# Kernel optimization log

Hardware: AMD Instinct MI355X
Metric: run time of the kernel (lower is better)

Reference implementation:

```python
import jax, jax.numpy as jnp
import numpy as np

N_NODES = 50000
N_EDGES = 800000
D = 128
E_DIM = 32
N_LAYERS = 4
BN_EPS = 1e-5


def setup_inputs() -> dict:
    key = jax.random.key(0)
    ks = jax.random.split(key, 9)
    return {
        "x": jax.random.normal(ks[0], (N_NODES, D), dtype=jnp.float32),
        "edge_attr": jax.random.normal(ks[1], (N_EDGES, E_DIM), dtype=jnp.float32),
        "edge_index": jax.random.randint(ks[2], (2, N_EDGES), 0, N_NODES, dtype=jnp.int64),
        "W_edge": jax.random.normal(ks[3], (N_LAYERS, E_DIM, D), dtype=jnp.float32) * 0.1,
        "b_edge": jnp.zeros((N_LAYERS, D), dtype=jnp.float32),
        "W1": jax.random.normal(ks[4], (N_LAYERS, D, D), dtype=jnp.float32) * 0.1,
        "b1": jnp.zeros((N_LAYERS, D), dtype=jnp.float32),
        "W2": jax.random.normal(ks[5], (N_LAYERS, D, D), dtype=jnp.float32) * 0.1,
        "b2": jnp.zeros((N_LAYERS, D), dtype=jnp.float32),
        "gamma": jnp.ones((N_LAYERS, D), dtype=jnp.float32),
        "beta": jnp.zeros((N_LAYERS, D), dtype=jnp.float32),
    }


def reference(x, edge_attr, edge_index, W_edge, b_edge, W1, b1, W2, b2, gamma, beta):
    src, dst = edge_index[0], edge_index[1]
    n = x.shape[0]
    for i in range(N_LAYERS):
        # GINEConv: message = ReLU(x_src + Lin(edge_attr)); scatter-add to dst
        e = edge_attr @ W_edge[i] + b_edge[i]            # [E, D]
        m = jax.nn.relu(x[src] + e)                      # [E, D]
        agg = jax.ops.segment_sum(m, dst, num_segments=n)  # [N, D]
        h = x + agg                                      # (1+eps)*x, eps=0
        # 2-layer MLP
        h = jax.nn.relu(h @ W1[i] + b1[i]) @ W2[i] + b2[i]
        # BatchNorm (training-mode batch stats, biased var) + ReLU; dropout off
        mean = h.mean(axis=0)
        var = h.var(axis=0)
        h = (h - mean) * jax.lax.rsqrt(var + BN_EPS) * gamma[i] + beta[i]
        x = jax.nn.relu(h)
    return x
```

## Files before the change

kernel.cpp:

```cpp
#include <hip/hip_runtime.h>

#define NN 50000
#define NE 800000
#define DD 128
#define ED 32
#define NL 4
#define BN_EPS 1e-5f
#define SCAN_B 1024
#define NB ((NN + SCAN_B - 1) / SCAN_B)
#define EB 128
#define MR 32

typedef __attribute__((ext_vector_type(8))) short bf16x8;
typedef __attribute__((ext_vector_type(4))) float f32x4;

__device__ __forceinline__ unsigned short f2bf(float f) {
    unsigned u = __float_as_uint(f);
    u += 0x7fffu + ((u >> 16) & 1u);
    return (unsigned short)(u >> 16);
}
__device__ __forceinline__ float bf2f(unsigned short h) {
    return __uint_as_float((unsigned)h << 16);
}

__global__ __launch_bounds__(256) void hist_kernel(
    const int* __restrict__ edst, int* __restrict__ deg)
{
    const int e = blockIdx.x * 256 + threadIdx.x;
    if (e < NE) atomicAdd(&deg[edst[e]], 1);
}

__global__ __launch_bounds__(256) void scan1_kernel(
    const int* __restrict__ deg, int* __restrict__ rowptr, int* __restrict__ bsum)
{
    __shared__ int sh[256];
    const int t = threadIdx.x, b = blockIdx.x;
    const int base = b * SCAN_B + t * 4;
    int v[4];
#pragma unroll
    for (int j = 0; j < 4; ++j) {
        const int idx = base + j;
        v[j] = (idx < NN) ? deg[idx] : 0;
    }
    sh[t] = v[0] + v[1] + v[2] + v[3];
    __syncthreads();
    for (int off = 1; off < 256; off <<= 1) {
        const int val = (t >= off) ? sh[t - off] : 0;
        __syncthreads();
        sh[t] += val;
        __syncthreads();
    }
    int p = (t == 0) ? 0 : sh[t - 1];
#pragma unroll
    for (int j = 0; j < 4; ++j) {
        const int idx = base + j;
        if (idx < NN) rowptr[idx] = p;
        p += v[j];
    }
    if (t == 255) bsum[b] = sh[255];
}

__global__ void scan2_kernel(int* __restrict__ bsum)
{
    if (threadIdx.x == 0) {
        int acc = 0;
        for (int i = 0; i < NB; ++i) { const int v = bsum[i]; bsum[i] = acc; acc += v; }
    }
}

__global__ __launch_bounds__(256) void scan3_kernel(
    int* __restrict__ rowptr, int* __restrict__ cursor, const int* __restrict__ bsum)
{
    const int idx = blockIdx.x * 256 + threadIdx.x;
    if (idx < NN) {
        const int v = rowptr[idx] + bsum[idx / SCAN_B];
        rowptr[idx] = v;
        cursor[idx] = v;
    }
    if (idx == 0) rowptr[NN] = NE;
}

__global__ __launch_bounds__(256) void scatter_idx_kernel(
    const int* __restrict__ edst, int* __restrict__ cursor, int* __restrict__ eid_perm)
{
    const int e = blockIdx.x * 256 + threadIdx.x;
    if (e < NE) {
        const int pos = atomicAdd(&cursor[edst[e]], 1);
        eid_perm[pos] = e;
    }
}

__global__ __launch_bounds__(256) void sdfill_kernel(
    const int* __restrict__ rowptr, const int* __restrict__ eid_perm,
    const int* __restrict__ esrc, int2* __restrict__ sd_perm)
{
    const int d = blockIdx.x * 256 + threadIdx.x;
    if (d < NN) {
        const int b = rowptr[d], e = rowptr[d + 1];
        for (int p = b; p < e; ++p)
            sd_perm[p] = make_int2(esrc[eid_perm[p]], d);
    }
}

__global__ __launch_bounds__(256) void ea_gather_kernel(
    const float* __restrict__ ea, const int* __restrict__ eid_perm,
    unsigned short* __restrict__ ea_bf)
{
    const int tid = blockIdx.x * 256 + threadIdx.x;
    const int pos = tid >> 3, j = tid & 7;
    if (pos < NE) {
        const int e = eid_perm[pos];
        const float4 v = *(const float4*)&ea[(size_t)e * ED + j * 4];
        uint2 p;
        p.x = (unsigned)f2bf(v.x) | ((unsigned)f2bf(v.y) << 16);
        p.y = (unsigned)f2bf(v.z) | ((unsigned)f2bf(v.w) << 16);
        *(uint2*)&ea_bf[(size_t)pos * ED + j * 4] = p;
    }
}

__global__ __launch_bounds__(256) void x0conv_kernel(
    const float* __restrict__ x0, unsigned short* __restrict__ xbf)
{
    const size_t i = ((size_t)blockIdx.x * 256 + threadIdx.x) * 8;
    if (i >= (size_t)NN * DD) return;
    const float4 a = *(const float4*)&x0[i];
    const float4 b = *(const float4*)&x0[i + 4];
    uint4 o;
    o.x = (unsigned)f2bf(a.x) | ((unsigned)f2bf(a.y) << 16);
    o.y = (unsigned)f2bf(a.z) | ((unsigned)f2bf(a.w) << 16);
    o.z = (unsigned)f2bf(b.x) | ((unsigned)f2bf(b.y) << 16);
    o.w = (unsigned)f2bf(b.z) | ((unsigned)f2bf(b.w) << 16);
    *(uint4*)&xbf[i] = o;
}

__global__ __launch_bounds__(256) void wconv_kernel(
    const float* __restrict__ We, unsigned short* __restrict__ wtb)
{
    const int tid = blockIdx.x * 256 + threadIdx.x;
    if (tid < NL * DD * ED) {
        const int l = tid / (DD * ED);
        const int r = tid % (DD * ED);
        const int c = r / ED, k = r % ED;
        wtb[tid] = f2bf(We[(size_t)l * ED * DD + k * DD + c]);
    }
}

__global__ __launch_bounds__(256) void w12conv_kernel(
    const float* __restrict__ W1, const float* __restrict__ W2,
    unsigned short* __restrict__ w1t, unsigned short* __restrict__ w2t)
{
    const int tid = blockIdx.x * 256 + threadIdx.x;
    if (tid < NL * DD * DD) {
        const int l = tid / (DD * DD);
        const int r = tid % (DD * DD);
        const int n = r / DD, k = r % DD;
        const size_t s = (size_t)l * DD * DD + k * DD + n;
        w1t[tid] = f2bf(W1[s]);
        w2t[tid] = f2bf(W2[s]);
    }
}

__global__ __launch_bounds__(256, 5) void edge_mfma_kernel(
    const unsigned short* __restrict__ xbf,
    const unsigned short* __restrict__ eab,
    const int2* __restrict__ sd_perm,
    const unsigned short* __restrict__ wtb,
    const float* __restrict__ be,
    float* __restrict__ agg)
{
    __shared__ unsigned short msgl[EB * 128];
    const int t = threadIdx.x;
    const int wv = t >> 6, ln = t & 63;
    const int l15 = ln & 15, kb = ln >> 4;
    const int e0 = blockIdx.x * EB;

    const int c0 = (2 * wv + 0) * 16 + l15;
    const int c1 = (2 * wv + 1) * 16 + l15;
    const bf16x8 bfr0 = *(const bf16x8*)&wtb[c0 * ED + kb * 8];
    const bf16x8 bfr1 = *(const bf16x8*)&wtb[c1 * ED + kb * 8];

#pragma unroll
    for (int eg = 0; eg < EB / 16; ++eg) {
        const int edge = eg * 16 + l15;
        const bf16x8 afr = *(const bf16x8*)&eab[(size_t)(e0 + edge) * ED + kb * 8];
        f32x4 z = {0.f, 0.f, 0.f, 0.f};
        const f32x4 d0 = __builtin_amdgcn_mfma_f32_16x16x32_bf16(afr, bfr0, z, 0, 0, 0);
        const f32x4 d1 = __builtin_amdgcn_mfma_f32_16x16x32_bf16(afr, bfr1, z, 0, 0, 0);
#pragma unroll
        for (int j = 0; j < 4; ++j) {
            const int mrow = eg * 16 + kb * 4 + j;
            const int sw = ((mrow >> 2) & 3) << 3;
            const int i0 = (((c0 >> 1) ^ sw) << 1) | (c0 & 1);
            const int i1 = (((c1 >> 1) ^ sw) << 1) | (c1 & 1);
            msgl[mrow * 128 + i0] = f2bf(d0[j]);
            msgl[mrow * 128 + i1] = f2bf(d1[j]);
        }
    }
    __syncthreads();

    const int lbase = wv * 32;
    const int2* sdp = &sd_perm[e0 + lbase];
    const int c2 = ln * 2;
    const float2 bv = *(const float2*)&be[c2];
    float2 acc = {0.f, 0.f};
    int seg_start = 0;
#pragma unroll 1
    for (int g = 0; g < 2; ++g) {
        const int gb = g * 16;
        int4 pr[8];
#pragma unroll
        for (int q = 0; q < 8; ++q)
            pr[q] = *(const int4*)&sdp[gb + 2 * q];
        int srcs[16], dsts[17];
#pragma unroll
        for (int q = 0; q < 8; ++q) {
            srcs[2 * q] = pr[q].x; srcs[2 * q + 1] = pr[q].z;
            dsts[2 * q] = pr[q].y; dsts[2 * q + 1] = pr[q].w;
        }
        dsts[16] = (gb + 16 < 32) ? sdp[gb + 16].y : -1;
        float2 xv[16];
#pragma unroll
        for (int q = 0; q < 16; ++q) {
            const unsigned xu = *(const unsigned*)&xbf[(size_t)srcs[q] * DD + c2];
            xv[q].x = __uint_as_float(xu << 16);
            xv[q].y = __uint_as_float(xu & 0xffff0000u);
        }
#pragma unroll
        for (int q = 0; q < 16; ++q) {
            const int i = gb + q;
            const int dw = ln ^ (((i >> 2) & 3) << 3);
            const unsigned mm = *(const unsigned*)&msgl[(lbase + i) * 128 + dw * 2];
            const float mlo = __uint_as_float(mm << 16);
            const float mhi = __uint_as_float(mm & 0xffff0000u);
            acc.x += fmaxf(xv[q].x + mlo + bv.x, 0.f);
            acc.y += fmaxf(xv[q].y + mhi + bv.y, 0.f);
            if (i == 31 || dsts[q + 1] != dsts[q]) {
                float* ap = &agg[(size_t)dsts[q] * DD + c2];
                if (seg_start > 0 && i < 31) {
                    *(float2*)ap = acc;
                } else {
                    unsafeAtomicAdd(ap + 0, acc.x);
                    unsafeAtomicAdd(ap + 1, acc.y);
                }
                acc.x = 0.f; acc.y = 0.f;
                seg_start = i + 1;
            }
        }
    }
}

__global__ __launch_bounds__(256, 5) void mlp_mfma_kernel(
    const unsigned short* __restrict__ xbf, const float* __restrict__ agg,
    float* __restrict__ h2out,
    const unsigned short* __restrict__ w1t,
    const unsigned short* __restrict__ w2t,
    const float* __restrict__ b1, const float* __restrict__ b2,
    float* __restrict__ bns)
{
    __shared__ unsigned short ah[MR * 128];
    __shared__ unsigned short al[MR * 128];
    __shared__ unsigned short bh[MR * 128];
    __shared__ unsigned short bl[MR * 128];
    const int t = threadIdx.x;
    const int wv = t >> 6, ln = t & 63, l15 = ln & 15, kb = ln >> 4;
    const int r0 = blockIdx.x * MR;

#pragma unroll
    for (int p = 0; p < 2; ++p) {
        const int row = p * 16 + (t >> 4);
        const int gc = t & 15;
        const int grow = r0 + row;
        float v[8] = {0.f, 0.f, 0.f, 0.f, 0.f, 0.f, 0.f, 0.f};
        if (grow < NN) {
            const size_t g = (size_t)grow * DD + gc * 8;
            const uint4 xu = *(const uint4*)&xbf[g];
            const float4 ga = *(const float4*)&agg[g];
            const float4 gb4 = *(const float4*)&agg[g + 4];
            v[0] = __uint_as_float(xu.x << 16)          + ga.x;
            v[1] = __uint_as_float(xu.x & 0xffff0000u)  + ga.y;
            v[2] = __uint_as_float(xu.y << 16)          + ga.z;
            v[3] = __uint_as_float(xu.y & 0xffff0000u)  + ga.w;
            v[4] = __uint_as_float(xu.z << 16)          + gb4.x;
            v[5] = __uint_as_float(xu.z & 0xffff0000u)  + gb4.y;
            v[6] = __uint_as_float(xu.w << 16)          + gb4.z;
            v[7] = __uint_as_float(xu.w & 0xffff0000u)  + gb4.w;
        }
        unsigned hiw[4], low[4];
#pragma unroll
        for (int j = 0; j < 4; ++j) {
            const unsigned short h0 = f2bf(v[2 * j]);
            const unsigned short h1 = f2bf(v[2 * j + 1]);
            const unsigned short q0 = f2bf(v[2 * j] - bf2f(h0));
            const unsigned short q1 = f2bf(v[2 * j + 1] - bf2f(h1));
            hiw[j] = (unsigned)h0 | ((unsigned)h1 << 16);
            low[j] = (unsigned)q0 | ((unsigned)q1 << 16);
        }
        const int off = row * 128 + (gc ^ (row & 7)) * 8;
        *(uint4*)&ah[off] = *(uint4*)hiw;
        *(uint4*)&al[off] = *(uint4*)low;
    }

    bf16x8 w1f[2][4];
#pragma unroll
    for (int nt = 0; nt < 2; ++nt) {
        const int n = wv * 32 + nt * 16 + l15;
#pragma unroll
        for (int ks = 0; ks < 4; ++ks)
            w1f[nt][ks] = *(const bf16x8*)&w1t[n * DD + ks * 32 + kb * 8];
    }
    const int cA = wv * 32 + l15, cB = wv * 32 + 16 + l15;
    const float b1v[2] = {b1[cA], b1[cB]};
    const float b2v[2] = {b2[cA], b2[cB]};
    __syncthreads();

    f32x4 acc[2][2];
#pragma unroll
    for (int mt = 0; mt < 2; ++mt)
#pragma unroll
        for (int nt = 0; nt < 2; ++nt)
            acc[mt][nt] = (f32x4){0.f, 0.f, 0.f, 0.f};
#pragma unroll
    for (int ks = 0; ks < 4; ++ks) {
#pragma unroll
        for (int mt = 0; mt < 2; ++mt) {
            const int row = mt * 16 + l15;
            const int off = row * 128 + ((ks * 4 + kb) ^ (row & 7)) * 8;
            const bf16x8 afh = *(const bf16x8*)&ah[off];
            const bf16x8 afl = *(const bf16x8*)&al[off];
#pragma unroll
            for (int nt = 0; nt < 2; ++nt) {
                acc[mt][nt] = __builtin_amdgcn_mfma_f32_16x16x32_bf16(afh, w1f[nt][ks], acc[mt][nt], 0, 0, 0);
                acc[mt][nt] = __builtin_amdgcn_mfma_f32_16x16x32_bf16(afl, w1f[nt][ks], acc[mt][nt], 0, 0, 0);
            }
        }
    }

#pragma unroll
    for (int mt = 0; mt < 2; ++mt) {
#pragma unroll
        for (int nt = 0; nt < 2; ++nt) {
            const int col = wv * 32 + nt * 16 + l15;
#pragma unroll
            for (int j = 0; j < 4; ++j) {
                const int row = mt * 16 + kb * 4 + j;
                const float v = fmaxf(acc[mt][nt][j] + b1v[nt], 0.f);
                const unsigned short hi = f2bf(v);
                const int off = row * 128 + ((col >> 3) ^ (row & 7)) * 8 + (col & 7);
                bh[off] = hi;
                bl[off] = f2bf(v - bf2f(hi));
            }
        }
    }

    bf16x8 w2f[2][4];
#pragma unroll
    for (int nt = 0; nt < 2; ++nt) {
        const int n = wv * 32 + nt * 16 + l15;
#pragma unroll
        for (int ks = 0; ks < 4; ++ks)
            w2f[nt][ks] = *(const bf16x8*)&w2t[n * DD + ks * 32 + kb * 8];
    }
    __syncthreads();

#pragma unroll
    for (int mt = 0; mt < 2; ++mt)
#pragma unroll
        for (int nt = 0; nt < 2; ++nt)
            acc[mt][nt] = (f32x4){0.f, 0.f, 0.f, 0.f};
#pragma unroll
    for (int ks = 0; ks < 4; ++ks) {
#pragma unroll
        for (int mt = 0; mt < 2; ++mt) {
            const int row = mt * 16 + l15;
            const int off = row * 128 + ((ks * 4 + kb) ^ (row & 7)) * 8;
            const bf16x8 afh = *(const bf16x8*)&bh[off];
            const bf16x8 afl = *(const bf16x8*)&bl[off];
#pragma unroll
            for (int nt = 0; nt < 2; ++nt) {
                acc[mt][nt] = __builtin_amdgcn_mfma_f32_16x16x32_bf16(afh, w2f[nt][ks], acc[mt][nt], 0, 0, 0);
                acc[mt][nt] = __builtin_amdgcn_mfma_f32_16x16x32_bf16(afl, w2f[nt][ks], acc[mt][nt], 0, 0, 0);
            }
        }
    }

    float ps[2] = {0.f, 0.f}, pq[2] = {0.f, 0.f};
#pragma unroll
    for (int mt = 0; mt < 2; ++mt) {
#pragma unroll
        for (int nt = 0; nt < 2; ++nt) {
            const int col = wv * 32 + nt * 16 + l15;
#pragma unroll
            for (int j = 0; j < 4; ++j) {
                const int row = r0 + mt * 16 + kb * 4 + j;
                const float v = acc[mt][nt][j] + b2v[nt];
                if (row < NN) {
                    h2out[(size_t)row * DD + col] = v;
                    ps[nt] += v;
                    pq[nt] += v * v;
                }
            }
        }
    }
#pragma unroll
    for (int nt = 0; nt < 2; ++nt) {
        ps[nt] += __shfl_xor(ps[nt], 16);
        ps[nt] += __shfl_xor(ps[nt], 32);
        pq[nt] += __shfl_xor(pq[nt], 16);
        pq[nt] += __shfl_xor(pq[nt], 32);
    }
    if (kb == 0) {
#pragma unroll
        for (int nt = 0; nt < 2; ++nt) {
            const int col = wv * 32 + nt * 16 + l15;
            unsafeAtomicAdd(&bns[col], ps[nt]);
            unsafeAtomicAdd(&bns[DD + col], pq[nt]);
        }
    }
}

__global__ __launch_bounds__(256) void bn_apply_bf16(
    float* __restrict__ h2, const float* __restrict__ bns,
    const float* __restrict__ gamma, const float* __restrict__ beta,
    unsigned short* __restrict__ xout)
{
    const size_t i = ((size_t)blockIdx.x * 256 + threadIdx.x) * 4;
    if (i >= (size_t)NN * DD) return;
    const int c4 = (int)(i & 127);
    const float4 hv = *(const float4*)&h2[i];
    const float4 sv = *(const float4*)&bns[c4];
    const float4 qv = *(const float4*)&bns[DD + c4];
    const float4 gv = *(const float4*)&gamma[c4];
    const float4 bv = *(const float4*)&beta[c4];
    const float inv_n = 1.f / (float)NN;
    float o0, o1, o2, o3;
    { const float m = sv.x * inv_n; const float var = qv.x * inv_n - m * m;
      o0 = fmaxf((hv.x - m) * __frsqrt_rn(var + BN_EPS) * gv.x + bv.x, 0.f); }
    { const float m = sv.y * inv_n; const float var = qv.y * inv_n - m * m;
      o1 = fmaxf((hv.y - m) * __frsqrt_rn(var + BN_EPS) * gv.y + bv.y, 0.f); }
    { const float m = sv.z * inv_n; const float var = qv.z * inv_n - m * m;
      o2 = fmaxf((hv.z - m) * __frsqrt_rn(var + BN_EPS) * gv.z + bv.z, 0.f); }
    { const float m = sv.w * inv_n; const float var = qv.w * inv_n - m * m;
      o3 = fmaxf((hv.w - m) * __frsqrt_rn(var + BN_EPS) * gv.w + bv.w, 0.f); }
    uint2 o;
    o.x = (unsigned)f2bf(o0) | ((unsigned)f2bf(o1) << 16);
    o.y = (unsigned)f2bf(o2) | ((unsigned)f2bf(o3) << 16);
    *(uint2*)&xout[i] = o;
    *(float4*)&h2[i] = (float4){0.f, 0.f, 0.f, 0.f};
}

__global__ __launch_bounds__(256) void bn_apply_f32(
    const float* __restrict__ h2, const float* __restrict__ bns,
    const float* __restrict__ gamma, const float* __restrict__ beta,
    float* __restrict__ xout)
{
    const size_t i = ((size_t)blockIdx.x * 256 + threadIdx.x) * 4;
    if (i >= (size_t)NN * DD) return;
    const int c4 = (int)(i & 127);
    const float4 hv = *(const float4*)&h2[i];
    const float4 sv = *(const float4*)&bns[c4];
    const float4 qv = *(const float4*)&bns[DD + c4];
    const float4 gv = *(const float4*)&gamma[c4];
    const float4 bv = *(const float4*)&beta[c4];
    const float inv_n = 1.f / (float)NN;
    float4 ov;
    { const float m = sv.x * inv_n; const float var = qv.x * inv_n - m * m;
      ov.x = fmaxf((hv.x - m) * __frsqrt_rn(var + BN_EPS) * gv.x + bv.x, 0.f); }
    { const float m = sv.y * inv_n; const float var = qv.y * inv_n - m * m;
      ov.y = fmaxf((hv.y - m) * __frsqrt_rn(var + BN_EPS) * gv.y + bv.y, 0.f); }
    { const float m = sv.z * inv_n; const float var = qv.z * inv_n - m * m;
      ov.z = fmaxf((hv.z - m) * __frsqrt_rn(var + BN_EPS) * gv.z + bv.z, 0.f); }
    { const float m = sv.w * inv_n; const float var = qv.w * inv_n - m * m;
      ov.w = fmaxf((hv.w - m) * __frsqrt_rn(var + BN_EPS) * gv.w + bv.w, 0.f); }
    *(float4*)&xout[i] = ov;
}

extern "C" void kernel_launch(void* const* d_in, const int* in_sizes, int n_in,
                              void* d_out, int out_size, void* d_ws, size_t ws_size,
                              hipStream_t stream) {
    const float* x0    = (const float*)d_in[0];
    const float* ea    = (const float*)d_in[1];
    const int*   eidx  = (const int*)d_in[2];
    const float* We    = (const float*)d_in[3];
    const float* be    = (const float*)d_in[4];
    const float* W1    = (const float*)d_in[5];
    const float* b1    = (const float*)d_in[6];
    const float* W2    = (const float*)d_in[7];
    const float* b2    = (const float*)d_in[8];
    const float* gamma = (const float*)d_in[9];
    const float* beta  = (const float*)d_in[10];
    float* out = (float*)d_out;
    float* ws  = (float*)d_ws;

    float* agg = ws;
    float* bns = agg + (size_t)NN * DD;
    int* deg      = (int*)(bns + NL * 256);
    int* rowptr   = deg + 50000;
    int* cursor   = rowptr + 50004;
    int* bsum     = cursor + 50000;
    int2* sd_perm = (int2*)(bsum + 64);
    int* eid_perm = (int*)(sd_perm + NE);
    unsigned short* ea_bf = (unsigned short*)(eid_perm + NE);
    unsigned short* wt_bf = ea_bf + (size_t)NE * ED;
    unsigned short* w1t   = wt_bf + (size_t)NL * DD * ED;
    unsigned short* w2t   = w1t + (size_t)NL * DD * DD;
    unsigned short* xbf   = w2t + (size_t)NL * DD * DD;

    const int* esrc = eidx;
    const int* edst = eidx + NE;

    hipMemsetAsync(deg, 0, NN * sizeof(int), stream);
    hipMemsetAsync(bns, 0, NL * 256 * sizeof(float), stream);
    hipMemsetAsync(agg, 0, (size_t)NN * DD * sizeof(float), stream);
    hist_kernel<<<(NE + 255) / 256, 256, 0, stream>>>(edst, deg);
    scan1_kernel<<<NB, 256, 0, stream>>>(deg, rowptr, bsum);
    scan2_kernel<<<1, 64, 0, stream>>>(bsum);
    scan3_kernel<<<(NN + 255) / 256, 256, 0, stream>>>(rowptr, cursor, bsum);
    scatter_idx_kernel<<<(NE + 255) / 256, 256, 0, stream>>>(edst, cursor, eid_perm);
    sdfill_kernel<<<(NN + 255) / 256, 256, 0, stream>>>(rowptr, eid_perm, esrc, sd_perm);
    ea_gather_kernel<<<(NE * 8 + 255) / 256, 256, 0, stream>>>(ea, eid_perm, ea_bf);
    x0conv_kernel<<<((NN * DD / 8) + 255) / 256, 256, 0, stream>>>(x0, xbf);
    wconv_kernel<<<(NL * DD * ED + 255) / 256, 256, 0, stream>>>(We, wt_bf);
    w12conv_kernel<<<(NL * DD * DD + 255) / 256, 256, 0, stream>>>(W1, W2, w1t, w2t);

    for (int l = 0; l < NL; ++l) {
        edge_mfma_kernel<<<NE / EB, 256, 0, stream>>>(
            xbf, ea_bf, sd_perm,
            wt_bf + (size_t)l * DD * ED, be + (size_t)l * DD, agg);
        mlp_mfma_kernel<<<(NN + MR - 1) / MR, 256, 0, stream>>>(
            xbf, agg, agg,
            w1t + (size_t)l * DD * DD, w2t + (size_t)l * DD * DD,
            b1 + (size_t)l * DD, b2 + (size_t)l * DD, bns + l * 256);
        if (l < NL - 1) {
            bn_apply_bf16<<<(NN * DD / 4 + 255) / 256, 256, 0, stream>>>(
                agg, bns + l * 256, gamma + (size_t)l * DD, beta + (size_t)l * DD, xbf);
        } else {
            bn_apply_f32<<<(NN * DD / 4 + 255) / 256, 256, 0, stream>>>(
                agg, bns + l * 256, gamma + (size_t)l * DD, beta + (size_t)l * DD, out);
        }
    }
}
```

Before: 650.3 us.

## Fuse edge preprocessing, batch all gathers in edge kernel, drop split-bf16 second GEMM

Merges the per-node sdfill loop and the ea_gather kernel into one per-edge kernel that writes the src/dst pairs and bf16 edge attributes, plus a sentinel entry past the end. The edge kernel now loads all 32 src/dst pairs and x gathers up front before accumulating, and its occupancy hint drops from 5 to 4. The MLP kernel stops using a hi/lo bf16 split of the hidden activations for the second GEMM, which halves those MFMAs and frees one shared-memory buffer at the cost of precision. The segment-flush logic is reworked to use the sentinel.

```diff
diff --git a/kernel.cpp b/kernel.cpp
--- a/kernel.cpp
+++ b/kernel.cpp
@@ -90,32 +90,27 @@
     }
 }
 
-__global__ __launch_bounds__(256) void sdfill_kernel(
-    const int* __restrict__ rowptr, const int* __restrict__ eid_perm,
-    const int* __restrict__ esrc, int2* __restrict__ sd_perm)
-{
-    const int d = blockIdx.x * 256 + threadIdx.x;
-    if (d < NN) {
-        const int b = rowptr[d], e = rowptr[d + 1];
-        for (int p = b; p < e; ++p)
-            sd_perm[p] = make_int2(esrc[eid_perm[p]], d);
-    }
-}
-
-__global__ __launch_bounds__(256) void ea_gather_kernel(
-    const float* __restrict__ ea, const int* __restrict__ eid_perm,
-    unsigned short* __restrict__ ea_bf)
-{
-    const int tid = blockIdx.x * 256 + threadIdx.x;
-    const int pos = tid >> 3, j = tid & 7;
+__global__ __launch_bounds__(256) void sdea_kernel(
+    const int* __restrict__ eid_perm, const int* __restrict__ esrc,
+    const int* __restrict__ edst, const float* __restrict__ ea,
+    int2* __restrict__ sd_perm, unsigned short* __restrict__ ea_bf)
+{
+    const int pos = blockIdx.x * 256 + threadIdx.x;
     if (pos < NE) {
         const int e = eid_perm[pos];
-        const float4 v = *(const float4*)&ea[(size_t)e * ED + j * 4];
-        uint2 p;
-        p.x = (unsigned)f2bf(v.x) | ((unsigned)f2bf(v.y) << 16);
-        p.y = (unsigned)f2bf(v.z) | ((unsigned)f2bf(v.w) << 16);
-        *(uint2*)&ea_bf[(size_t)pos * ED + j * 4] = p;
-    }
+        sd_perm[pos] = make_int2(esrc[e], edst[e]);
+        const float* er = &ea[(size_t)e * ED];
+        unsigned short* ob = &ea_bf[(size_t)pos * ED];
+#pragma unroll
+        for (int g = 0; g < 8; ++g) {
+            const float4 v = *(const float4*)&er[g * 4];
+            uint2 p;
+            p.x = (unsigned)f2bf(v.x) | ((unsigned)f2bf(v.y) << 16);
+            p.y = (unsigned)f2bf(v.z) | ((unsigned)f2bf(v.w) << 16);
+            *(uint2*)&ob[g * 4] = p;
+        }
+    }
+    if (pos == 0) sd_perm[NE] = make_int2(0, -1);
 }
 
 __global__ __launch_bounds__(256) void x0conv_kernel(
@@ -160,7 +155,7 @@
     }
 }
 
-__global__ __launch_bounds__(256, 5) void edge_mfma_kernel(
+__global__ __launch_bounds__(256, 4) void edge_mfma_kernel(
     const unsigned short* __restrict__ xbf,
     const unsigned short* __restrict__ eab,
     const int2* __restrict__ sd_perm,
@@ -202,48 +197,48 @@
     const int2* sdp = &sd_perm[e0 + lbase];
     const int c2 = ln * 2;
     const float2 bv = *(const float2*)&be[c2];
-    float2 acc = {0.f, 0.f};
-    int seg_start = 0;
-#pragma unroll 1
-    for (int g = 0; g < 2; ++g) {
-        const int gb = g * 16;
-        int4 pr[8];
-#pragma unroll
-        for (int q = 0; q < 8; ++q)
-            pr[q] = *(const int4*)&sdp[gb + 2 * q];
-        int srcs[16], dsts[17];
-#pragma unroll
-        for (int q = 0; q < 8; ++q) {
-            srcs[2 * q] = pr[q].x; srcs[2 * q + 1] = pr[q].z;
-            dsts[2 * q] = pr[q].y; dsts[2 * q + 1] = pr[q].w;
-        }
-        dsts[16] = (gb + 16 < 32) ? sdp[gb + 16].y : -1;
-        float2 xv[16];
+
+    int4 pr[16];
+#pragma unroll
+    for (int q = 0; q < 16; ++q)
+        pr[q] = *(const int4*)&sdp[2 * q];
+    int dsts[33];
+#pragma unroll
+    for (int q = 0; q < 16; ++q) {
+        dsts[2 * q]     = pr[q].y;
+        dsts[2 * q + 1] = pr[q].w;
+    }
+    dsts[32] = sdp[32].y;
+    unsigned xu[32];
+#pragma unroll
+    for (int q = 0; q < 16; ++q) {
+        xu[2 * q]     = *(const unsigned*)&xbf[(size_t)pr[q].x * DD + c2];
+        xu[2 * q + 1] = *(const unsigned*)&xbf[(size_t)pr[q].z * DD + c2];
+    }
+
+#pragma unroll
+    for (int h = 0; h < 2; ++h) {
+        float2 acc = {0.f, 0.f};
+        int segfirst = 1;
 #pragma unroll
         for (int q = 0; q < 16; ++q) {
-            const unsigned xu = *(const unsigned*)&xbf[(size_t)srcs[q] * DD + c2];
-            xv[q].x = __uint_as_float(xu << 16);
-            xv[q].y = __uint_as_float(xu & 0xffff0000u);
-        }
-#pragma unroll
-        for (int q = 0; q < 16; ++q) {
-            const int i = gb + q;
+            const int i = h * 16 + q;
             const int dw = ln ^ (((i >> 2) & 3) << 3);
             const unsigned mm = *(const unsigned*)&msgl[(lbase + i) * 128 + dw * 2];
             const float mlo = __uint_as_float(mm << 16);
             const float mhi = __uint_as_float(mm & 0xffff0000u);
-            acc.x += fmaxf(xv[q].x + mlo + bv.x, 0.f);
-            acc.y += fmaxf(xv[q].y + mhi + bv.y, 0.f);
-            if (i == 31 || dsts[q + 1] != dsts[q]) {
-                float* ap = &agg[(size_t)dsts[q] * DD + c2];
-                if (seg_start > 0 && i < 31) {
+            acc.x += fmaxf(__uint_as_float(xu[i] << 16) + mlo + bv.x, 0.f);
+            acc.y += fmaxf(__uint_as_float(xu[i] & 0xffff0000u) + mhi + bv.y, 0.f);
+            if (q == 15 || dsts[i + 1] != dsts[i]) {
+                float* ap = &agg[(size_t)dsts[i] * DD + c2];
+                if (!segfirst && dsts[i + 1] != dsts[i]) {
                     *(float2*)ap = acc;
                 } else {
                     unsafeAtomicAdd(ap + 0, acc.x);
                     unsafeAtomicAdd(ap + 1, acc.y);
                 }
                 acc.x = 0.f; acc.y = 0.f;
-                seg_start = i + 1;
+                segfirst = 0;
             }
         }
     }
@@ -260,7 +255,6 @@
     __shared__ unsigned short ah[MR * 128];
     __shared__ unsigned short al[MR * 128];
     __shared__ unsigned short bh[MR * 128];
-    __shared__ unsigned short bl[MR * 128];
     const int t = threadIdx.x;
     const int wv = t >> 6, ln = t & 63, l15 = ln & 15, kb = ln >> 4;
     const int r0 = blockIdx.x * MR;
@@ -344,10 +338,8 @@
             for (int j = 0; j < 4; ++j) {
                 const int row = mt * 16 + kb * 4 + j;
                 const float v = fmaxf(acc[mt][nt][j] + b1v[nt], 0.f);
-                const unsigned short hi = f2bf(v);
                 const int off = row * 128 + ((col >> 3) ^ (row & 7)) * 8 + (col & 7);
-                bh[off] = hi;
-                bl[off] = f2bf(v - bf2f(hi));
+                bh[off] = f2bf(v);
             }
         }
     }
@@ -374,12 +366,9 @@
             const int row = mt * 16 + l15;
             const int off = row * 128 + ((ks * 4 + kb) ^ (row & 7)) * 8;
             const bf16x8 afh = *(const bf16x8*)&bh[off];
-            const bf16x8 afl = *(const bf16x8*)&bl[off];
-#pragma unroll
-            for (int nt = 0; nt < 2; ++nt) {
+#pragma unroll
+            for (int nt = 0; nt < 2; ++nt)
                 acc[mt][nt] = __builtin_amdgcn_mfma_f32_16x16x32_bf16(afh, w2f[nt][ks], acc[mt][nt], 0, 0, 0);
-                acc[mt][nt] = __builtin_amdgcn_mfma_f32_16x16x32_bf16(afl, w2f[nt][ks], acc[mt][nt], 0, 0, 0);
-            }
         }
     }
 
@@ -498,7 +487,7 @@
     int* cursor   = rowptr + 50004;
     int* bsum     = cursor + 50000;
     int2* sd_perm = (int2*)(bsum + 64);
-    int* eid_perm = (int*)(sd_perm + NE);
+    int* eid_perm = (int*)(sd_perm + NE + 2);
     unsigned short* ea_bf = (unsigned short*)(eid_perm + NE);
     unsigned short* wt_bf = ea_bf + (size_t)NE * ED;
     unsigned short* w1t   = wt_bf + (size_t)NL * DD * ED;
@@ -516,8 +505,8 @@
     scan2_kernel<<<1, 64, 0, stream>>>(bsum);
     scan3_kernel<<<(NN + 255) / 256, 256, 0, stream>>>(rowptr, cursor, bsum);
     scatter_idx_kernel<<<(NE + 255) / 256, 256, 0, stream>>>(edst, cursor, eid_perm);
-    sdfill_kernel<<<(NN + 255) / 256, 256, 0, stream>>>(rowptr, eid_perm, esrc, sd_perm);
-    ea_gather_kernel<<<(NE * 8 + 255) / 256, 256, 0, stream>>>(ea, eid_perm, ea_bf);
+    sdea_kernel<<<(NE + 255) / 256, 256, 0, stream>>>(
+        eid_perm, esrc, edst, ea, sd_perm, ea_bf);
     x0conv_kernel<<<((NN * DD / 8) + 255) / 256, 256, 0, stream>>>(x0, xbf);
     wconv_kernel<<<(NL * DD * ED + 255) / 256, 256, 0, stream>>>(We, wt_bf);
     w12conv_kernel<<<(NL * DD * DD + 255) / 256, 256, 0, stream>>>(W1, W2, w1t, w2t);
```

Measured after the change: 800.0 us. 1.23x slower.
